# Performance work log

Measured on AMD Instinct MI355X. Metric: run time of the kernel, lower is better.

The kernel has to match this reference:

```python
import jax, jax.numpy as jnp
import numpy as np

B, S, D = 2, 2048, 2560
H, DH = 32, 80           # heads, head_size = D // H
RD = 32                  # rotary_dim (partial RoPE)
NI = 10240               # n_inner = 4 * n_embd
EPS = 1e-5
ROPE_BASE = 10000.0


def setup_inputs() -> dict:
    key = jax.random.key(0)
    ks = jax.random.split(key, 12)
    sd = 0.02
    inp = {
        "position_ids": jnp.broadcast_to(jnp.arange(S, dtype=jnp.int64), (B, S)),
        "hidden_states": jax.random.normal(ks[0], (B, S, D), jnp.float32),
        "ln_g": jnp.ones((D,), jnp.float32),
        "ln_b": jnp.zeros((D,), jnp.float32),
        "wqkv": jax.random.normal(ks[1], (D, 3 * D), jnp.float32) * sd,
        "bqkv": jnp.zeros((3 * D,), jnp.float32),
        "wout": jax.random.normal(ks[2], (D, D), jnp.float32) * sd,
        "bout": jnp.zeros((D,), jnp.float32),
        "wfc1": jax.random.normal(ks[3], (D, NI), jnp.float32) * sd,
        "bfc1": jnp.zeros((NI,), jnp.float32),
        "wfc2": jax.random.normal(ks[4], (NI, D), jnp.float32) * sd,
        "bfc2": jnp.zeros((D,), jnp.float32),
    }
    return inp


def _rope_neox(x, positions):
    # x: [B,S,H,DH]; apply neox-style rotary to first RD dims only
    half = RD // 2
    inv_freq = 1.0 / (ROPE_BASE ** (jnp.arange(0, RD, 2, dtype=jnp.float32) / RD))  # [half]
    ang = positions.astype(jnp.float32)[..., None] * inv_freq                        # [B,S,half]
    cos = jnp.cos(ang)[:, :, None, :]  # [B,S,1,half]
    sin = jnp.sin(ang)[:, :, None, :]
    x1 = x[..., :half]
    x2 = x[..., half:RD]
    rot = jnp.concatenate([x1 * cos - x2 * sin, x2 * cos + x1 * sin], axis=-1)
    return jnp.concatenate([rot, x[..., RD:]], axis=-1)


def reference(position_ids, hidden_states, ln_g, ln_b, wqkv, bqkv, wout, bout,
              wfc1, bfc1, wfc2, bfc2):
    residual = hidden_states
    # LayerNorm
    mu = jnp.mean(hidden_states, axis=-1, keepdims=True)
    var = jnp.mean(jnp.square(hidden_states - mu), axis=-1, keepdims=True)
    x = (hidden_states - mu) * jax.lax.rsqrt(var + EPS) * ln_g + ln_b

    # QKV projection
    qkv = x @ wqkv + bqkv
    q, k, v = jnp.split(qkv, 3, axis=-1)
    q = q.reshape(B, S, H, DH)
    k = k.reshape(B, S, H, DH)
    v = v.reshape(B, S, H, DH)

    # partial RoPE (neox style) on q and k
    q = _rope_neox(q, position_ids)
    k = _rope_neox(k, position_ids)

    # causal attention
    scale = DH ** -0.5
    scores = jnp.einsum("bqhd,bkhd->bhqk", q, k) * scale
    causal = jnp.tril(jnp.ones((S, S), jnp.bool_))
    scores = jnp.where(causal, scores, jnp.finfo(scores.dtype).min)
    probs = jax.nn.softmax(scores, axis=-1)
    attn = jnp.einsum("bhqk,bkhd->bqhd", probs, v).reshape(B, S, D)
    attn_out = attn @ wout + bout

    # MLP (gelu_new = tanh-approx gelu) on the SAME normed x (parallel residual)
    mlp = jax.nn.gelu(x @ wfc1 + bfc1, approximate=True) @ wfc2 + bfc2

    return attn_out + mlp + residual
```

## Files before the change

### kernel.cpp

```cpp
#include <hip/hip_runtime.h>

#define SS   2048
#define DD   2560
#define HH   32
#define DHH  80
#define DPAD 96
#define NII  10240
#define NTOK 4096

typedef __attribute__((ext_vector_type(8))) __bf16 bf16x8;
typedef __attribute__((ext_vector_type(4))) float  f32x4;

__device__ __forceinline__ float bf2f(unsigned short h) {
  union { unsigned u; float f; } c; c.u = ((unsigned)h) << 16; return c.f;
}
__device__ __forceinline__ unsigned short f2bf(float f) {
  union { float f; unsigned u; } c; c.f = f;
  unsigned r = c.u + 0x7FFFu + ((c.u >> 16) & 1u);
  return (unsigned short)(r >> 16);
}

__device__ __forceinline__ void gl_lds16(const void* gptr, void* lptr) {
  __builtin_amdgcn_global_load_lds((__attribute__((address_space(1))) void*)gptr,
                                   (__attribute__((address_space(3))) void*)lptr,
                                   16, 0, 0);
}

__global__ __launch_bounds__(256) void wt_transpose(const float* __restrict__ W,
                                                    unsigned short* __restrict__ Wt,
                                                    int K, int N) {
  __shared__ float tile[32][33];
  const int tx = threadIdx.x & 31, ty = threadIdx.x >> 5;
  const int n0 = blockIdx.x * 32, k0 = blockIdx.y * 32;
#pragma unroll
  for (int i = 0; i < 32; i += 8)
    tile[ty + i][tx] = W[(size_t)(k0 + ty + i) * N + n0 + tx];
  __syncthreads();
#pragma unroll
  for (int i = 0; i < 32; i += 8)
    Wt[(size_t)(n0 + ty + i) * K + k0 + tx] = f2bf(tile[tx][ty + i]);
}

__global__ __launch_bounds__(256) void ln_kernel(const float* __restrict__ X,
                                                 const float* __restrict__ G,
                                                 const float* __restrict__ Bb,
                                                 unsigned short* __restrict__ Xo) {
  const int row = blockIdx.x;
  const float4* xr = (const float4*)(X + (size_t)row * DD);
  float s = 0.f, ss = 0.f;
  for (int i = threadIdx.x; i < DD / 4; i += 256) {
    float4 v = xr[i];
    s  += v.x + v.y + v.z + v.w;
    ss += v.x * v.x + v.y * v.y + v.z * v.z + v.w * v.w;
  }
#pragma unroll
  for (int o = 32; o > 0; o >>= 1) { s += __shfl_down(s, o, 64); ss += __shfl_down(ss, o, 64); }
  __shared__ float red[8];
  const int w = threadIdx.x >> 6;
  if ((threadIdx.x & 63) == 0) { red[w] = s; red[4 + w] = ss; }
  __syncthreads();
  if (threadIdx.x == 0) {
    float ts  = red[0] + red[1] + red[2] + red[3];
    float tss = red[4] + red[5] + red[6] + red[7];
    float mu  = ts * (1.f / DD);
    float var = tss * (1.f / DD) - mu * mu;
    red[0] = mu; red[1] = rsqrtf(var + 1e-5f);
  }
  __syncthreads();
  const float mu = red[0], rstd = red[1];
  const float4* gr = (const float4*)G;
  const float4* br = (const float4*)Bb;
  for (int i = threadIdx.x; i < DD / 4; i += 256) {
    float4 v = xr[i], g = gr[i], b = br[i];
    ushort4 o;
    o.x = f2bf((v.x - mu) * rstd * g.x + b.x);
    o.y = f2bf((v.y - mu) * rstd * g.y + b.y);
    o.z = f2bf((v.z - mu) * rstd * g.z + b.z);
    o.w = f2bf((v.w - mu) * rstd * g.w + b.w);
    *(ushort4*)&Xo[(size_t)row * DD + i * 4] = o;
  }
}

__global__ __launch_bounds__(256) void rope_kernel(const unsigned short* __restrict__ qkv,
                                                   unsigned short* __restrict__ Qp,
                                                   unsigned short* __restrict__ Kp,
                                                   unsigned short* __restrict__ Vt) {
  const int tok = blockIdx.x;
  const int b = tok / SS, s = tok % SS;
  __shared__ float cs[16], sn[16];
  if (threadIdx.x < 16) {
    float inv = powf(10000.f, -(float)threadIdx.x / 16.f);
    float ang = (float)s * inv;
    cs[threadIdx.x] = cosf(ang);
    sn[threadIdx.x] = sinf(ang);
  }
  __syncthreads();
  const unsigned short* row = qkv + (size_t)tok * (3 * DD);
  for (int idx = threadIdx.x; idx < 2 * HH * DPAD; idx += 256) {
    const int which = idx / (HH * DPAD);
    const int rrem  = idx % (HH * DPAD);
    const int h = rrem / DPAD, d = rrem % DPAD;
    float val = 0.f;
    if (d < DHH) {
      const unsigned short* base = row + which * DD + h * DHH;
      if (d < 16) {
        float x1 = bf2f(base[d]), x2 = bf2f(base[d + 16]);
        val = x1 * cs[d] - x2 * sn[d];
      } else if (d < 32) {
        int i2 = d - 16;
        float x1 = bf2f(base[i2]), x2 = bf2f(base[d]);
        val = x2 * cs[i2] + x1 * sn[i2];
      } else {
        val = bf2f(base[d]);
      }
    }
    unsigned short* outp = which ? Kp : Qp;
    outp[(((size_t)b * HH + h) * SS + s) * DPAD + d] = f2bf(val);
  }
  for (int idx = threadIdx.x; idx < DD; idx += 256) {
    const int h = idx / DHH, d = idx % DHH;
    Vt[(((size_t)b * HH + h) * DHH + d) * SS + s] = row[2 * DD + idx];
  }
}

__global__ __launch_bounds__(128) void attn_kernel(const unsigned short* __restrict__ Qp,
                                                   const unsigned short* __restrict__ Kp,
                                                   const unsigned short* __restrict__ Vt,
                                                   unsigned short* __restrict__ O) {
  const int bid = blockIdx.x;
  const int bh = bid & 63;
  const int p = 63 - (bid >> 6);
  const int w = threadIdx.x >> 6;
  const int tile = p * 2 + w;
  const int lane = threadIdx.x & 63;
  const int lr = lane & 15, lg = lane >> 4;
  const int q0 = tile * 16;
  const unsigned short* Qh = Qp + (size_t)bh * SS * DPAD;
  const unsigned short* Kh = Kp + (size_t)bh * SS * DPAD;
  const unsigned short* Vh = Vt + (size_t)bh * DHH * SS;
  __shared__ __align__(16) char Plds[2][2048];
  char* Pb = Plds[w];

  bf16x8 qf[3];
#pragma unroll
  for (int c = 0; c < 3; ++c)
    qf[c] = *(const bf16x8*)&Qh[(size_t)(q0 + lr) * DPAD + c * 32 + lg * 8];

  f32x4 oacc[5];
#pragma unroll
  for (int d = 0; d < 5; ++d) oacc[d] = (f32x4){0.f, 0.f, 0.f, 0.f};
  float mrow[4], lrow[4];
#pragma unroll
  for (int r = 0; r < 4; ++r) { mrow[r] = -1e30f; lrow[r] = 0.f; }

  const float scl = 0.11180339887498949f;
  const int nt = q0 / 64 + 1;
  for (int t = 0; t < nt; ++t) {
    const int kv0 = t * 64;
    f32x4 s0 = (f32x4){0.f, 0.f, 0.f, 0.f};
    f32x4 s1 = (f32x4){0.f, 0.f, 0.f, 0.f};
    f32x4 s2 = (f32x4){0.f, 0.f, 0.f, 0.f};
    f32x4 s3 = (f32x4){0.f, 0.f, 0.f, 0.f};
#pragma unroll
    for (int c = 0; c < 3; ++c) {
      bf16x8 k0 = *(const bf16x8*)&Kh[(size_t)(kv0 +      lr) * DPAD + c * 32 + lg * 8];
      bf16x8 k1 = *(const bf16x8*)&Kh[(size_t)(kv0 + 16 + lr) * DPAD + c * 32 + lg * 8];
      bf16x8 k2 = *(const bf16x8*)&Kh[(size_t)(kv0 + 32 + lr) * DPAD + c * 32 + lg * 8];
      bf16x8 k3 = *(const bf16x8*)&Kh[(size_t)(kv0 + 48 + lr) * DPAD + c * 32 + lg * 8];
      s0 = __builtin_amdgcn_mfma_f32_16x16x32_bf16(qf[c], k0, s0, 0, 0, 0);
      s1 = __builtin_amdgcn_mfma_f32_16x16x32_bf16(qf[c], k1, s1, 0, 0, 0);
      s2 = __builtin_amdgcn_mfma_f32_16x16x32_bf16(qf[c], k2, s2, 0, 0, 0);
      s3 = __builtin_amdgcn_mfma_f32_16x16x32_bf16(qf[c], k3, s3, 0, 0, 0);
    }
    float pv0[4], pv1[4], pv2[4], pv3[4], mx[4];
    bool need = false;
#pragma unroll
    for (int r = 0; r < 4; ++r) {
      const int qr = q0 + lg * 4 + r;
      float a0 = (kv0 +      lr > qr) ? -1e30f : s0[r] * scl;
      float a1 = (kv0 + 16 + lr > qr) ? -1e30f : s1[r] * scl;
      float a2 = (kv0 + 32 + lr > qr) ? -1e30f : s2[r] * scl;
      float a3 = (kv0 + 48 + lr > qr) ? -1e30f : s3[r] * scl;
      pv0[r] = a0; pv1[r] = a1; pv2[r] = a2; pv3[r] = a3;
      float m = fmaxf(fmaxf(a0, a1), fmaxf(a2, a3));
#pragma unroll
      for (int mk = 1; mk < 16; mk <<= 1) m = fmaxf(m, __shfl_xor(m, mk, 64));
      mx[r] = m;
      need = need || (m > mrow[r] + 8.f);
    }
    if (__ballot(need)) {
#pragma unroll
      for (int r = 0; r < 4; ++r) {
        float mnew = fmaxf(mrow[r], mx[r]);
        float resc = __expf(mrow[r] - mnew);
        lrow[r] *= resc;
#pragma unroll
        for (int d = 0; d < 5; ++d) oacc[d][r] *= resc;
        mrow[r] = mnew;
      }
    }
#pragma unroll
    for (int r = 0; r < 4; ++r) {
      const int row = lg * 4 + r;
      const int swz = (row & 7) << 4;
      float p0 = __expf(pv0[r] - mrow[r]);
      float p1 = __expf(pv1[r] - mrow[r]);
      float p2 = __expf(pv2[r] - mrow[r]);
      float p3 = __expf(pv3[r] - mrow[r]);
      *(unsigned short*)(Pb + row * 128 + ((( 0 + lr) * 2) ^ swz)) = f2bf(p0);
      *(unsigned short*)(Pb + row * 128 + (((16 + lr) * 2) ^ swz)) = f2bf(p1);
      *(unsigned short*)(Pb + row * 128 + (((32 + lr) * 2) ^ swz)) = f2bf(p2);
      *(unsigned short*)(Pb + row * 128 + (((48 + lr) * 2) ^ swz)) = f2bf(p3);
      float rs = (p0 + p1) + (p2 + p3);
#pragma unroll
      for (int mk = 1; mk < 16; mk <<= 1) rs += __shfl_xor(rs, mk, 64);
      lrow[r] += rs;
    }
    asm volatile("s_waitcnt lgkmcnt(0)" ::: "memory");
    const int rswz = (lr & 7) << 4;
    bf16x8 pa0 = *(const bf16x8*)(Pb + lr * 128 + ((lg * 16) ^ rswz));
    bf16x8 pa1 = *(const bf16x8*)(Pb + lr * 128 + ((64 + lg * 16) ^ rswz));
#pragma unroll
    for (int d = 0; d < 5; ++d) {
      bf16x8 v0 = *(const bf16x8*)&Vh[(size_t)(d * 16 + lr) * SS + kv0 + lg * 8];
      bf16x8 v1 = *(const bf16x8*)&Vh[(size_t)(d * 16 + lr) * SS + kv0 + 32 + lg * 8];
      oacc[d] = __builtin_amdgcn_mfma_f32_16x16x32_bf16(pa0, v0, oacc[d], 0, 0, 0);
      oacc[d] = __builtin_amdgcn_mfma_f32_16x16x32_bf16(pa1, v1, oacc[d], 0, 0, 0);
    }
  }
  const int b = bh >> 5, h = bh & 31;
#pragma unroll
  for (int r = 0; r < 4; ++r) {
    const int qr = q0 + lg * 4 + r;
    const float inv = 1.f / lrow[r];
#pragma unroll
    for (int d = 0; d < 5; ++d)
      O[(size_t)(b * SS + qr) * DD + h * DHH + d * 16 + lr] = f2bf(oacc[d][r] * inv);
  }
}

__device__ __forceinline__ float gelu_f(float x) {
  float x3 = x * x * x;
  return 0.5f * x * (1.f + tanhf(0.7978845608028654f * (x + 0.044715f * x3)));
}

template <int MODE>
__global__ __launch_bounds__(512, 2) void gemm256(const unsigned short* __restrict__ A,
                                                  const unsigned short* __restrict__ Bt,
                                                  const float* __restrict__ bias,
                                                  void* __restrict__ Cout,
                                                  const unsigned short* __restrict__ addb,
                                                  const float* __restrict__ addf,
                                                  int M, int N, int K, int nby) {
  __shared__ __align__(16) char lds[131072];

  const int bid = blockIdx.x;
  const int by = bid % nby, bx = bid / nby;
  const int m0 = by * 256, n0 = bx * 256;

  const int tid = threadIdx.x;
  const int w = tid >> 6, lane = tid & 63;
  const int lr = lane & 15, lg = lane >> 4;
  const int wm = w >> 2, wn = w & 3;

  const int srow = w * 16 + (lane >> 3);
  const int scol = ((lane & 7) ^ ((lane >> 3) & 7)) * 8;
  const unsigned short* pA = A  + (size_t)(m0 + srow) * K + scol;
  const unsigned short* pB = Bt + (size_t)(n0 + srow) * K + scol;
  const int wdst = w * 2048;

  const int rdA = wm * 16384 + lr * 128;
  const int rdB = 65536 + (wn >> 1) * 16384 + ((wn & 1) * 64 + lr) * 128;
  const int sl0 = ((lg) ^ (lr & 7)) << 4;
  const int sl1 = ((4 + lg) ^ (lr & 7)) << 4;

  f32x4 acc[8][4];
#pragma unroll
  for (int i = 0; i < 8; ++i)
#pragma unroll
    for (int j = 0; j < 4; ++j) acc[i][j] = (f32x4){0.f, 0.f, 0.f, 0.f};

  const int nt = K >> 6;

#define RA(BUF, m, kh) (*(const bf16x8*)(lds + (BUF) + rdA + (m) * 2048 + ((kh) ? sl1 : sl0)))
#define RB(BUF, n, kh) (*(const bf16x8*)(lds + (BUF) + rdB + (n) * 2048 + ((kh) ? sl1 : sl0)))
#define STGA(dt, h, DST)                                                       \
  { const unsigned short* s_ = pA + (size_t)(dt) * 64 + (size_t)(h) * 128 * K; \
    gl_lds16(s_,                 lds + (DST) + wdst);                          \
    gl_lds16(s_ + (size_t)8 * K, lds + (DST) + wdst + 1024); }
#define STGB(dt, h, DST)                                                       \
  { const unsigned short* s_ = pB + (size_t)(dt) * 64 + (size_t)(h) * 128 * K; \
    gl_lds16(s_,                 lds + 65536 + (DST) + wdst);                  \
    gl_lds16(s_ + (size_t)8 * K, lds + 65536 + (DST) + wdst + 1024); }
#define BARR __builtin_amdgcn_s_barrier()
#define MFMA8x2(AV, BV, MB, NB)                                              \
  __builtin_amdgcn_s_setprio(1);                                             \
  _Pragma("unroll") for (int kh_ = 0; kh_ < 2; ++kh_)                        \
  _Pragma("unroll") for (int m_ = 0; m_ < 4; ++m_)                           \
  _Pragma("unroll") for (int n_ = 0; n_ < 2; ++n_)                           \
    acc[(MB) + m_][(NB) + n_] = __builtin_amdgcn_mfma_f32_16x16x32_bf16(     \
        AV[m_][kh_], BV[n_][kh_], acc[(MB) + m_][(NB) + n_], 0, 0, 0);       \
  __builtin_amdgcn_s_setprio(0);

  STGA(0, 0, 0);
  STGA(0, 1, 16384);
  STGB(0, 0, 0);
  STGB(0, 1, 16384);
  STGA(1, 0, 32768);
  STGA(1, 1, 32768 + 16384);
  STGB(1, 0, 32768);
  asm volatile("s_waitcnt vmcnt(6)" ::: "memory");
  BARR;
  __builtin_amdgcn_sched_barrier(0);

  for (int t = 0; t < nt; t += 2) {
    const bool more = (t + 2 < nt);
    bf16x8 avL[4][2], avH[4][2], bvL[2][2], bvH[2][2];

#pragma unroll
    for (int m_ = 0; m_ < 4; ++m_) { avL[m_][0] = RA(0, m_, 0); avL[m_][1] = RA(0, m_, 1); }
#pragma unroll
    for (int n_ = 0; n_ < 2; ++n_) { bvL[n_][0] = RB(0, n_, 0); bvL[n_][1] = RB(0, n_, 1); }
    STGB(1, 1, 32768 + 16384);
    BARR;
    MFMA8x2(avL, bvL, 0, 0);
    BARR;
#pragma unroll
    for (int m_ = 0; m_ < 4; ++m_) { avH[m_][0] = RA(0, 4 + m_, 0); avH[m_][1] = RA(0, 4 + m_, 1); }
    BARR;
    MFMA8x2(avH, bvL, 4, 0);
    BARR;
#pragma unroll
    for (int n_ = 0; n_ < 2; ++n_) { bvH[n_][0] = RB(0, 2 + n_, 0); bvH[n_][1] = RB(0, 2 + n_, 1); }
    if (more) STGA(2, 0, 0);
    BARR;
    MFMA8x2(avH, bvH, 4, 2);
    BARR;
    if (more) STGA(2, 1, 16384);
    BARR;
    MFMA8x2(avL, bvH, 0, 2);
    if (more) { asm volatile("s_waitcnt vmcnt(4)" ::: "memory"); }
    else      { asm volatile("s_waitcnt vmcnt(0)" ::: "memory"); }
    BARR;
    __builtin_amdgcn_sched_barrier(0);

#pragma unroll
    for (int m_ = 0; m_ < 4; ++m_) { avL[m_][0] = RA(32768, m_, 0); avL[m_][1] = RA(32768, m_, 1); }
#pragma unroll
    for (int n_ = 0; n_ < 2; ++n_) { bvL[n_][0] = RB(32768, n_, 0); bvL[n_][1] = RB(32768, n_, 1); }
    if (more) STGB(2, 0, 0);
    BARR;
    MFMA8x2(avL, bvL, 0, 0);
    BARR;
#pragma unroll
    for (int m_ = 0; m_ < 4; ++m_) { avH[m_][0] = RA(32768, 4 + m_, 0); avH[m_][1] = RA(32768, 4 + m_, 1); }
    if (more) STGB(2, 1, 16384);
    BARR;
    MFMA8x2(avH, bvL, 4, 0);
    BARR;
#pragma unroll
    for (int n_ = 0; n_ < 2; ++n_) { bvH[n_][0] = RB(32768, 2 + n_, 0); bvH[n_][1] = RB(32768, 2 + n_, 1); }
    if (more) STGA(3, 0, 32768);
    BARR;
    MFMA8x2(avH, bvH, 4, 2);
    BARR;
    if (more) { STGA(3, 1, 32768 + 16384); STGB(3, 0, 32768); }
    BARR;
    MFMA8x2(avL, bvH, 0, 2);
    if (more) { asm volatile("s_waitcnt vmcnt(6)" ::: "memory"); }
    BARR;
    __builtin_amdgcn_sched_barrier(0);

    pA += 128; pB += 128;
  }
#undef RA
#undef RB
#undef STGA
#undef STGB
#undef BARR
#undef MFMA8x2

#pragma unroll
  for (int m = 0; m < 8; ++m) {
    const int rb = m0 + wm * 128 + m * 16 + lg * 4;
#pragma unroll
    for (int n = 0; n < 4; ++n) {
      const int col = n0 + wn * 64 + n * 16 + lr;
      const float bv = bias[col];
#pragma unroll
      for (int r = 0; r < 4; ++r) {
        const size_t idx = (size_t)(rb + r) * N + col;
        float v = acc[m][n][r] + bv;
        if (MODE == 2) v = gelu_f(v);
        if (MODE == 3) {
          ((float*)Cout)[idx] = v + bf2f(addb[idx]) + addf[idx];
        } else {
          ((unsigned short*)Cout)[idx] = f2bf(v);
        }
      }
    }
  }
}

extern "C" void kernel_launch(void* const* d_in, const int* in_sizes, int n_in,
                              void* d_out, int out_size, void* d_ws, size_t ws_size,
                              hipStream_t stream) {
  (void)in_sizes; (void)n_in; (void)out_size; (void)ws_size;
  const float* hidden = (const float*)d_in[1];
  const float* ln_g = (const float*)d_in[2];
  const float* ln_b = (const float*)d_in[3];
  const float* wqkv = (const float*)d_in[4];
  const float* bqkv = (const float*)d_in[5];
  const float* wout = (const float*)d_in[6];
  const float* bout = (const float*)d_in[7];
  const float* wfc1 = (const float*)d_in[8];
  const float* bfc1 = (const float*)d_in[9];
  const float* wfc2 = (const float*)d_in[10];
  const float* bfc2 = (const float*)d_in[11];
  float* out = (float*)d_out;

  char* ws = (char*)d_ws;
  size_t off = 0;
  auto alloc = [&](size_t bytes) -> void* {
    void* p = ws + off;
    off += (bytes + 255) & ~(size_t)255;
    return p;
  };
  unsigned short* wqkvT = (unsigned short*)alloc((size_t)3 * DD * DD * 2);
  unsigned short* woutT = (unsigned short*)alloc((size_t)DD * DD * 2);
  unsigned short* wfc1T = (unsigned short*)alloc((size_t)NII * DD * 2);
  unsigned short* wfc2T = (unsigned short*)alloc((size_t)DD * NII * 2);
  unsigned short* xln   = (unsigned short*)alloc((size_t)NTOK * DD * 2);
  unsigned short* regA  = (unsigned short*)alloc((size_t)NTOK * NII * 2);
  unsigned short* Qp    = (unsigned short*)alloc((size_t)2 * HH * SS * DPAD * 2);
  unsigned short* Kp    = (unsigned short*)alloc((size_t)2 * HH * SS * DPAD * 2);
  unsigned short* Vt    = (unsigned short*)alloc((size_t)2 * HH * DHH * SS * 2);
  unsigned short* Obuf  = (unsigned short*)alloc((size_t)NTOK * DD * 2);
  unsigned short* qkvbuf   = regA;
  unsigned short* h1       = regA;
  unsigned short* attnproj = Qp;

  wt_transpose<<<dim3(3 * DD / 32, DD / 32), 256, 0, stream>>>(wqkv, wqkvT, DD, 3 * DD);
  wt_transpose<<<dim3(DD / 32, DD / 32), 256, 0, stream>>>(wout, woutT, DD, DD);
  wt_transpose<<<dim3(NII / 32, DD / 32), 256, 0, stream>>>(wfc1, wfc1T, DD, NII);
  wt_transpose<<<dim3(DD / 32, NII / 32), 256, 0, stream>>>(wfc2, wfc2T, NII, DD);
  ln_kernel<<<NTOK, 256, 0, stream>>>(hidden, ln_g, ln_b, xln);
  gemm256<0><<<dim3((3 * DD / 256) * (NTOK / 256)), 512, 0, stream>>>(
      xln, wqkvT, bqkv, qkvbuf, nullptr, nullptr, NTOK, 3 * DD, DD, NTOK / 256);
  rope_kernel<<<NTOK, 256, 0, stream>>>(qkvbuf, Qp, Kp, Vt);
  attn_kernel<<<dim3(4096), 128, 0, stream>>>(Qp, Kp, Vt, Obuf);
  gemm256<0><<<dim3((DD / 256) * (NTOK / 256)), 512, 0, stream>>>(
      Obuf, woutT, bout, attnproj, nullptr, nullptr, NTOK, DD, DD, NTOK / 256);
  gemm256<2><<<dim3((NII / 256) * (NTOK / 256)), 512, 0, stream>>>(
      xln, wfc1T, bfc1, h1, nullptr, nullptr, NTOK, NII, DD, NTOK / 256);
  gemm256<3><<<dim3((DD / 256) * (NTOK / 256)), 512, 0, stream>>>(
      h1, wfc2T, bfc2, out, attnproj, hidden, NTOK, DD, NII, NTOK / 256);
}
```

Measured before the change: 1.302 ms.

## Quantize QKV and output projection GEMMs to int8 with per-row/column scales

Replaces the bf16 QKV and attention-output projection GEMMs with an int8 MFMA GEMM. Weights get per-output-column absmax scales and activations get per-row absmax scales, with dequantization folded into the epilogue. This targets double-rate int8 matrix throughput and halves operand bandwidth. It adds colmax, quantize and rowquant passes and lowers numerical accuracy, which the tolerance may not accept.

```diff
diff --git a/kernel.cpp b/kernel.cpp
--- a/kernel.cpp
+++ b/kernel.cpp
@@ -10,6 +10,7 @@
 
 typedef __attribute__((ext_vector_type(8))) __bf16 bf16x8;
 typedef __attribute__((ext_vector_type(4))) float  f32x4;
+typedef __attribute__((ext_vector_type(4))) int    i32x4;
 
 __device__ __forceinline__ float bf2f(unsigned short h) {
   union { unsigned u; float f; } c; c.u = ((unsigned)h) << 16; return c.f;
@@ -24,6 +25,17 @@
   __builtin_amdgcn_global_load_lds((__attribute__((address_space(1))) void*)gptr,
                                    (__attribute__((address_space(3))) void*)lptr,
                                    16, 0, 0);
+}
+
+__global__ __launch_bounds__(256) void colmax_kernel(const float* __restrict__ W,
+                                                     float* __restrict__ rawmax,
+                                                     int K, int N) {
+  const int n = blockIdx.x * 256 + threadIdx.x;
+  const int kc = K >> 3;
+  const int k0 = blockIdx.y * kc, k1 = k0 + kc;
+  float m = 0.f;
+  for (int k = k0; k < k1; ++k) m = fmaxf(m, fabsf(W[(size_t)k * N + n]));
+  atomicMax((unsigned*)&rawmax[n], __float_as_uint(m));
 }
 
 __global__ __launch_bounds__(256) void wt_transpose(const float* __restrict__ W,
@@ -39,6 +51,65 @@
 #pragma unroll
   for (int i = 0; i < 32; i += 8)
     Wt[(size_t)(n0 + ty + i) * K + k0 + tx] = f2bf(tile[tx][ty + i]);
+}
+
+__global__ __launch_bounds__(256) void wt_q8(const float* __restrict__ W,
+                                             signed char* __restrict__ Wt8,
+                                             const float* __restrict__ rawmax,
+                                             int K, int N) {
+  __shared__ float tile[32][33];
+  const int tx = threadIdx.x & 31, ty = threadIdx.x >> 5;
+  const int n0 = blockIdx.x * 32, k0 = blockIdx.y * 32;
+#pragma unroll
+  for (int i = 0; i < 32; i += 8)
+    tile[ty + i][tx] = W[(size_t)(k0 + ty + i) * N + n0 + tx];
+  __syncthreads();
+#pragma unroll
+  for (int i = 0; i < 32; i += 8) {
+    const int n = n0 + ty + i;
+    const float inv = 127.f / fmaxf(rawmax[n], 1e-20f);
+    float q = rintf(tile[tx][ty + i] * inv);
+    q = fminf(fmaxf(q, -127.f), 127.f);
+    Wt8[(size_t)n * K + k0 + tx] = (signed char)q;
+  }
+}
+
+__global__ __launch_bounds__(256) void rowquant(const unsigned short* __restrict__ in,
+                                                signed char* __restrict__ outq,
+                                                float* __restrict__ srow, int Kd) {
+  const int row = blockIdx.x;
+  const unsigned short* r = in + (size_t)row * Kd;
+  float m = 0.f;
+  for (int i = threadIdx.x; i < Kd / 4; i += 256) {
+    ushort4 v = *(const ushort4*)&r[i * 4];
+    m = fmaxf(m, fabsf(bf2f(v.x)));
+    m = fmaxf(m, fabsf(bf2f(v.y)));
+    m = fmaxf(m, fabsf(bf2f(v.z)));
+    m = fmaxf(m, fabsf(bf2f(v.w)));
+  }
+#pragma unroll
+  for (int o = 32; o > 0; o >>= 1) m = fmaxf(m, __shfl_down(m, o, 64));
+  __shared__ float red[4];
+  if ((threadIdx.x & 63) == 0) red[threadIdx.x >> 6] = m;
+  __syncthreads();
+  if (threadIdx.x == 0) {
+    float t = fmaxf(fmaxf(red[0], red[1]), fmaxf(red[2], red[3]));
+    t = fmaxf(t, 1e-20f);
+    red[0] = 127.f / t;
+    srow[row] = t / 127.f;
+  }
+  __syncthreads();
+  const float inv = red[0];
+  signed char* o = outq + (size_t)row * Kd;
+  for (int i = threadIdx.x; i < Kd / 4; i += 256) {
+    ushort4 v = *(const ushort4*)&r[i * 4];
+    char4 q;
+    q.x = (signed char)fminf(fmaxf(rintf(bf2f(v.x) * inv), -127.f), 127.f);
+    q.y = (signed char)fminf(fmaxf(rintf(bf2f(v.y) * inv), -127.f), 127.f);
+    q.z = (signed char)fminf(fmaxf(rintf(bf2f(v.z) * inv), -127.f), 127.f);
+    q.w = (signed char)fminf(fmaxf(rintf(bf2f(v.w) * inv), -127.f), 127.f);
+    *(char4*)&o[i * 4] = q;
+  }
 }
 
 __global__ __launch_bounds__(256) void ln_kernel(const float* __restrict__ X,
@@ -402,6 +473,158 @@
   }
 }
 
+__global__ __launch_bounds__(512, 2) void gemm256_i8(const signed char* __restrict__ A,
+                                                     const signed char* __restrict__ Bt,
+                                                     const float* __restrict__ sA,
+                                                     const float* __restrict__ rawB,
+                                                     const float* __restrict__ bias,
+                                                     unsigned short* __restrict__ Cout,
+                                                     int M, int N, int K, int nby) {
+  __shared__ __align__(16) char lds[131072];
+
+  const int bid = blockIdx.x;
+  const int by = bid % nby, bx = bid / nby;
+  const int m0 = by * 256, n0 = bx * 256;
+
+  const int tid = threadIdx.x;
+  const int w = tid >> 6, lane = tid & 63;
+  const int lr = lane & 15, lg = lane >> 4;
+  const int wm = w >> 2, wn = w & 3;
+
+  const int srow = w * 16 + (lane >> 3);
+  const int scol = ((lane & 7) ^ ((lane >> 3) & 7)) * 16;
+  const signed char* pA = A  + (size_t)(m0 + srow) * K + scol;
+  const signed char* pB = Bt + (size_t)(n0 + srow) * K + scol;
+  const int wdst = w * 2048;
+
+  const int rdA = wm * 16384 + lr * 128;
+  const int rdB = 65536 + (wn >> 1) * 16384 + ((wn & 1) * 64 + lr) * 128;
+  const int sl0 = ((lg) ^ (lr & 7)) << 4;
+  const int sl1 = ((4 + lg) ^ (lr & 7)) << 4;
+
+  i32x4 acc[8][4];
+#pragma unroll
+  for (int i = 0; i < 8; ++i)
+#pragma unroll
+    for (int j = 0; j < 4; ++j) acc[i][j] = (i32x4){0, 0, 0, 0};
+
+  const int nt = K >> 7;
+
+#define RAI(BUF, m, kh) (*(const i32x4*)(lds + (BUF) + rdA + (m) * 2048 + ((kh) ? sl1 : sl0)))
+#define RBI(BUF, n, kh) (*(const i32x4*)(lds + (BUF) + rdB + (n) * 2048 + ((kh) ? sl1 : sl0)))
+#define STGAI(dt, h, DST)                                                       \
+  { const signed char* s_ = pA + (size_t)(dt) * 128 + (size_t)(h) * 128 * K;    \
+    gl_lds16(s_,                 lds + (DST) + wdst);                           \
+    gl_lds16(s_ + (size_t)8 * K, lds + (DST) + wdst + 1024); }
+#define STGBI(dt, h, DST)                                                       \
+  { const signed char* s_ = pB + (size_t)(dt) * 128 + (size_t)(h) * 128 * K;    \
+    gl_lds16(s_,                 lds + 65536 + (DST) + wdst);                   \
+    gl_lds16(s_ + (size_t)8 * K, lds + 65536 + (DST) + wdst + 1024); }
+#define BARRI __builtin_amdgcn_s_barrier()
+#define MFMAI8x2(AV, BV, MB, NB)                                             \
+  __builtin_amdgcn_s_setprio(1);                                             \
+  _Pragma("unroll") for (int kh_ = 0; kh_ < 2; ++kh_)                        \
+  _Pragma("unroll") for (int m_ = 0; m_ < 4; ++m_)                           \
+  _Pragma("unroll") for (int n_ = 0; n_ < 2; ++n_)                           \
+    acc[(MB) + m_][(NB) + n_] = __builtin_amdgcn_mfma_i32_16x16x64_i8(       \
+        AV[m_][kh_], BV[n_][kh_], acc[(MB) + m_][(NB) + n_], 0, 0, 0);       \
+  __builtin_amdgcn_s_setprio(0);
+
+  STGAI(0, 0, 0);
+  STGAI(0, 1, 16384);
+  STGBI(0, 0, 0);
+  STGBI(0, 1, 16384);
+  STGAI(1, 0, 32768);
+  STGAI(1, 1, 32768 + 16384);
+  STGBI(1, 0, 32768);
+  asm volatile("s_waitcnt vmcnt(6)" ::: "memory");
+  BARRI;
+  __builtin_amdgcn_sched_barrier(0);
+
+  for (int t = 0; t < nt; t += 2) {
+    const bool more = (t + 2 < nt);
+    i32x4 avL[4][2], avH[4][2], bvL[2][2], bvH[2][2];
+
+#pragma unroll
+    for (int m_ = 0; m_ < 4; ++m_) { avL[m_][0] = RAI(0, m_, 0); avL[m_][1] = RAI(0, m_, 1); }
+#pragma unroll
+    for (int n_ = 0; n_ < 2; ++n_) { bvL[n_][0] = RBI(0, n_, 0); bvL[n_][1] = RBI(0, n_, 1); }
+    STGBI(1, 1, 32768 + 16384);
+    BARRI;
+    MFMAI8x2(avL, bvL, 0, 0);
+    BARRI;
+#pragma unroll
+    for (int m_ = 0; m_ < 4; ++m_) { avH[m_][0] = RAI(0, 4 + m_, 0); avH[m_][1] = RAI(0, 4 + m_, 1); }
+    BARRI;
+    MFMAI8x2(avH, bvL, 4, 0);
+    BARRI;
+#pragma unroll
+    for (int n_ = 0; n_ < 2; ++n_) { bvH[n_][0] = RBI(0, 2 + n_, 0); bvH[n_][1] = RBI(0, 2 + n_, 1); }
+    if (more) STGAI(2, 0, 0);
+    BARRI;
+    MFMAI8x2(avH, bvH, 4, 2);
+    BARRI;
+    if (more) STGAI(2, 1, 16384);
+    BARRI;
+    MFMAI8x2(avL, bvH, 0, 2);
+    if (more) { asm volatile("s_waitcnt vmcnt(4)" ::: "memory"); }
+    else      { asm volatile("s_waitcnt vmcnt(0)" ::: "memory"); }
+    BARRI;
+    __builtin_amdgcn_sched_barrier(0);
+
+#pragma unroll
+    for (int m_ = 0; m_ < 4; ++m_) { avL[m_][0] = RAI(32768, m_, 0); avL[m_][1] = RAI(32768, m_, 1); }
+#pragma unroll
+    for (int n_ = 0; n_ < 2; ++n_) { bvL[n_][0] = RBI(32768, n_, 0); bvL[n_][1] = RBI(32768, n_, 1); }
+    if (more) STGBI(2, 0, 0);
+    BARRI;
+    MFMAI8x2(avL, bvL, 0, 0);
+    BARRI;
+#pragma unroll
+    for (int m_ = 0; m_ < 4; ++m_) { avH[m_][0] = RAI(32768, 4 + m_, 0); avH[m_][1] = RAI(32768, 4 + m_, 1); }
+    if (more) STGBI(2, 1, 16384);
+    BARRI;
+    MFMAI8x2(avH, bvL, 4, 0);
+    BARRI;
+#pragma unroll
+    for (int n_ = 0; n_ < 2; ++n_) { bvH[n_][0] = RBI(32768, 2 + n_, 0); bvH[n_][1] = RBI(32768, 2 + n_, 1); }
+    if (more) STGAI(3, 0, 32768);
+    BARRI;
+    MFMAI8x2(avH, bvH, 4, 2);
+    BARRI;
+    if (more) { STGAI(3, 1, 32768 + 16384); STGBI(3, 0, 32768); }
+    BARRI;
+    MFMAI8x2(avL, bvH, 0, 2);
+    if (more) { asm volatile("s_waitcnt vmcnt(6)" ::: "memory"); }
+    BARRI;
+    __builtin_amdgcn_sched_barrier(0);
+
+    pA += 256; pB += 256;
+  }
+#undef RAI
+#undef RBI
+#undef STGAI
+#undef STGBI
+#undef BARRI
+#undef MFMAI8x2
+
+#pragma unroll
+  for (int m = 0; m < 8; ++m) {
+    const int rb = m0 + wm * 128 + m * 16 + lg * 4;
+    float sr0 = sA[rb], sr1 = sA[rb + 1], sr2 = sA[rb + 2], sr3 = sA[rb + 3];
+#pragma unroll
+    for (int n = 0; n < 4; ++n) {
+      const int col = n0 + wn * 64 + n * 16 + lr;
+      const float sc = rawB[col] * (1.f / 127.f);
+      const float bv = bias[col];
+      Cout[(size_t)(rb + 0) * N + col] = f2bf((float)acc[m][n][0] * sr0 * sc + bv);
+      Cout[(size_t)(rb + 1) * N + col] = f2bf((float)acc[m][n][1] * sr1 * sc + bv);
+      Cout[(size_t)(rb + 2) * N + col] = f2bf((float)acc[m][n][2] * sr2 * sc + bv);
+      Cout[(size_t)(rb + 3) * N + col] = f2bf((float)acc[m][n][3] * sr3 * sc + bv);
+    }
+  }
+}
+
 extern "C" void kernel_launch(void* const* d_in, const int* in_sizes, int n_in,
                               void* d_out, int out_size, void* d_ws, size_t ws_size,
                               hipStream_t stream) {
@@ -426,11 +649,17 @@
     off += (bytes + 255) & ~(size_t)255;
     return p;
   };
-  unsigned short* wqkvT = (unsigned short*)alloc((size_t)3 * DD * DD * 2);
-  unsigned short* woutT = (unsigned short*)alloc((size_t)DD * DD * 2);
+  signed char*  wqkvT8 = (signed char*)alloc((size_t)3 * DD * DD);
+  signed char*  woutT8 = (signed char*)alloc((size_t)DD * DD);
   unsigned short* wfc1T = (unsigned short*)alloc((size_t)NII * DD * 2);
   unsigned short* wfc2T = (unsigned short*)alloc((size_t)DD * NII * 2);
   unsigned short* xln   = (unsigned short*)alloc((size_t)NTOK * DD * 2);
+  signed char*  xq      = (signed char*)alloc((size_t)NTOK * DD);
+  signed char*  oq      = (signed char*)alloc((size_t)NTOK * DD);
+  float* rawqkv = (float*)alloc((size_t)3 * DD * 4);
+  float* rawout = (float*)alloc((size_t)DD * 4);
+  float* sx     = (float*)alloc((size_t)NTOK * 4);
+  float* so     = (float*)alloc((size_t)NTOK * 4);
   unsigned short* regA  = (unsigned short*)alloc((size_t)NTOK * NII * 2);
   unsigned short* Qp    = (unsigned short*)alloc((size_t)2 * HH * SS * DPAD * 2);
   unsigned short* Kp    = (unsigned short*)alloc((size_t)2 * HH * SS * DPAD * 2);
@@ -440,17 +669,23 @@
   unsigned short* h1       = regA;
   unsigned short* attnproj = Qp;
 
-  wt_transpose<<<dim3(3 * DD / 32, DD / 32), 256, 0, stream>>>(wqkv, wqkvT, DD, 3 * DD);
-  wt_transpose<<<dim3(DD / 32, DD / 32), 256, 0, stream>>>(wout, woutT, DD, DD);
+  hipMemsetAsync(rawqkv, 0, (size_t)(3 * DD + DD) * 4, stream);
+
+  colmax_kernel<<<dim3(3 * DD / 256, 8), 256, 0, stream>>>(wqkv, rawqkv, DD, 3 * DD);
+  colmax_kernel<<<dim3(DD / 256, 8), 256, 0, stream>>>(wout, rawout, DD, DD);
+  wt_q8<<<dim3(3 * DD / 32, DD / 32), 256, 0, stream>>>(wqkv, wqkvT8, rawqkv, DD, 3 * DD);
+  wt_q8<<<dim3(DD / 32, DD / 32), 256, 0, stream>>>(wout, woutT8, rawout, DD, DD);
   wt_transpose<<<dim3(NII / 32, DD / 32), 256, 0, stream>>>(wfc1, wfc1T, DD, NII);
   wt_transpose<<<dim3(DD / 32, NII / 32), 256, 0, stream>>>(wfc2, wfc2T, NII, DD);
   ln_kernel<<<NTOK, 256, 0, stream>>>(hidden, ln_g, ln_b, xln);
-  gemm256<0><<<dim3((3 * DD / 256) * (NTOK / 256)), 512, 0, stream>>>(
-      xln, wqkvT, bqkv, qkvbuf, nullptr, nullptr, NTOK, 3 * DD, DD, NTOK / 256);
+  rowquant<<<NTOK, 256, 0, stream>>>(xln, xq, sx, DD);
+  gemm256_i8<<<dim3((3 * DD / 256) * (NTOK / 256)), 512, 0, stream>>>(
+      xq, wqkvT8, sx, rawqkv, bqkv, qkvbuf, NTOK, 3 * DD, DD, NTOK / 256);
   rope_kernel<<<NTOK, 256, 0, stream>>>(qkvbuf, Qp, Kp, Vt);
   attn_kernel<<<dim3(4096), 128, 0, stream>>>(Qp, Kp, Vt, Obuf);
-  gemm256<0><<<dim3((DD / 256) * (NTOK / 256)), 512, 0, stream>>>(
-      Obuf, woutT, bout, attnproj, nullptr, nullptr, NTOK, DD, DD, NTOK / 256);
+  rowquant<<<NTOK, 256, 0, stream>>>(Obuf, oq, so, DD);
+  gemm256_i8<<<dim3((DD / 256) * (NTOK / 256)), 512, 0, stream>>>(
+      oq, woutT8, so, rawout, bout, attnproj, NTOK, DD, DD, NTOK / 256);
   gemm256<2><<<dim3((NII / 256) * (NTOK / 256)), 512, 0, stream>>>(
       xln, wfc1T, bfc1, h1, nullptr, nullptr, NTOK, NII, DD, NTOK / 256);
   gemm256<3><<<dim3((DD / 256) * (NTOK / 256)), 512, 0, stream>>>(
```

Result: slower. 1.487 ms (+14.2%).

## Replace direct global-to-LDS loads with register-staged double-buffered GEMM pipeline

Applied to the files above, without the earlier changes.

The GEMM main loop stops using global_load_lds with a hand-scheduled barrier and vmcnt pipeline. Instead it loads the next K-tile into registers, stores it to a swizzled, double-buffered LDS slot, and synchronises with __syncthreads around each tile's MFMA work. Launch bounds drop to one block per CU, which gives more registers for the staging buffers. This simplifies scheduling but adds VGPR pressure and an LDS write pass, and it may lose the fine-grained overlap of the original interleaved schedule.

```diff
diff --git a/kernel.cpp b/kernel.cpp
--- a/kernel.cpp
+++ b/kernel.cpp
@@ -18,12 +18,6 @@
   union { float f; unsigned u; } c; c.f = f;
   unsigned r = c.u + 0x7FFFu + ((c.u >> 16) & 1u);
   return (unsigned short)(r >> 16);
-}
-
-__device__ __forceinline__ void gl_lds16(const void* gptr, void* lptr) {
-  __builtin_amdgcn_global_load_lds((__attribute__((address_space(1))) void*)gptr,
-                                   (__attribute__((address_space(3))) void*)lptr,
-                                   16, 0, 0);
 }
 
 __global__ __launch_bounds__(256) void wt_transpose(const float* __restrict__ W,
@@ -245,7 +239,7 @@
 }
 
 template <int MODE>
-__global__ __launch_bounds__(512, 2) void gemm256(const unsigned short* __restrict__ A,
+__global__ __launch_bounds__(512, 1) void gemm256(const unsigned short* __restrict__ A,
                                                   const unsigned short* __restrict__ Bt,
                                                   const float* __restrict__ bias,
                                                   void* __restrict__ Cout,
@@ -263,14 +257,20 @@
   const int lr = lane & 15, lg = lane >> 4;
   const int wm = w >> 2, wn = w & 3;
 
-  const int srow = w * 16 + (lane >> 3);
-  const int scol = ((lane & 7) ^ ((lane >> 3) & 7)) * 8;
-  const unsigned short* pA = A  + (size_t)(m0 + srow) * K + scol;
-  const unsigned short* pB = Bt + (size_t)(n0 + srow) * K + scol;
-  const int wdst = w * 2048;
+  const int srow = w * 32 + (lane >> 3);
+  const int sslot = lane & 7;
+  const unsigned short* pA = A  + (size_t)(m0 + srow) * K + sslot * 8;
+  const unsigned short* pB = Bt + (size_t)(n0 + srow) * K + sslot * 8;
+
+  int wadr[4];
+#pragma unroll
+  for (int i = 0; i < 4; ++i) {
+    const int row = srow + i * 8;
+    wadr[i] = (row >> 7) * 16384 + (row & 127) * 128 + ((sslot ^ (row & 7)) << 4);
+  }
 
   const int rdA = wm * 16384 + lr * 128;
-  const int rdB = 65536 + (wn >> 1) * 16384 + ((wn & 1) * 64 + lr) * 128;
+  const int rdB = (wn >> 1) * 16384 + ((wn & 1) * 64 + lr) * 128;
   const int sl0 = ((lg) ^ (lr & 7)) << 4;
   const int sl1 = ((4 + lg) ^ (lr & 7)) << 4;
 
@@ -282,17 +282,16 @@
 
   const int nt = K >> 6;
 
-#define RA(BUF, m, kh) (*(const bf16x8*)(lds + (BUF) + rdA + (m) * 2048 + ((kh) ? sl1 : sl0)))
-#define RB(BUF, n, kh) (*(const bf16x8*)(lds + (BUF) + rdB + (n) * 2048 + ((kh) ? sl1 : sl0)))
-#define STGA(dt, h, DST)                                                       \
-  { const unsigned short* s_ = pA + (size_t)(dt) * 64 + (size_t)(h) * 128 * K; \
-    gl_lds16(s_,                 lds + (DST) + wdst);                          \
-    gl_lds16(s_ + (size_t)8 * K, lds + (DST) + wdst + 1024); }
-#define STGB(dt, h, DST)                                                       \
-  { const unsigned short* s_ = pB + (size_t)(dt) * 64 + (size_t)(h) * 128 * K; \
-    gl_lds16(s_,                 lds + 65536 + (DST) + wdst);                  \
-    gl_lds16(s_ + (size_t)8 * K, lds + 65536 + (DST) + wdst + 1024); }
-#define BARR __builtin_amdgcn_s_barrier()
+  bf16x8 ra[4], rb[4];
+
+#define ISSUE(t)                                                        \
+  { const unsigned short* qa = pA + (size_t)(t) * 64;                   \
+    const unsigned short* qb = pB + (size_t)(t) * 64;                   \
+    _Pragma("unroll") for (int i = 0; i < 4; ++i) {                     \
+      ra[i] = *(const bf16x8*)(qa + (size_t)i * 8 * K);                 \
+      rb[i] = *(const bf16x8*)(qb + (size_t)i * 8 * K); } }
+#define RA(AB, m, kh) (*(const bf16x8*)(lds + (AB) + rdA + (m) * 2048 + ((kh) ? sl1 : sl0)))
+#define RB(BB, n, kh) (*(const bf16x8*)(lds + (BB) + rdB + (n) * 2048 + ((kh) ? sl1 : sl0)))
 #define MFMA8x2(AV, BV, MB, NB)                                              \
   __builtin_amdgcn_s_setprio(1);                                             \
   _Pragma("unroll") for (int kh_ = 0; kh_ < 2; ++kh_)                        \
@@ -302,94 +301,49 @@
         AV[m_][kh_], BV[n_][kh_], acc[(MB) + m_][(NB) + n_], 0, 0, 0);       \
   __builtin_amdgcn_s_setprio(0);
 
-  STGA(0, 0, 0);
-  STGA(0, 1, 16384);
-  STGB(0, 0, 0);
-  STGB(0, 1, 16384);
-  STGA(1, 0, 32768);
-  STGA(1, 1, 32768 + 16384);
-  STGB(1, 0, 32768);
-  asm volatile("s_waitcnt vmcnt(6)" ::: "memory");
-  BARR;
-  __builtin_amdgcn_sched_barrier(0);
-
-  for (int t = 0; t < nt; t += 2) {
-    const bool more = (t + 2 < nt);
-    bf16x8 avL[4][2], avH[4][2], bvL[2][2], bvH[2][2];
-
-#pragma unroll
-    for (int m_ = 0; m_ < 4; ++m_) { avL[m_][0] = RA(0, m_, 0); avL[m_][1] = RA(0, m_, 1); }
-#pragma unroll
-    for (int n_ = 0; n_ < 2; ++n_) { bvL[n_][0] = RB(0, n_, 0); bvL[n_][1] = RB(0, n_, 1); }
-    STGB(1, 1, 32768 + 16384);
-    BARR;
-    MFMA8x2(avL, bvL, 0, 0);
-    BARR;
-#pragma unroll
-    for (int m_ = 0; m_ < 4; ++m_) { avH[m_][0] = RA(0, 4 + m_, 0); avH[m_][1] = RA(0, 4 + m_, 1); }
-    BARR;
-    MFMA8x2(avH, bvL, 4, 0);
-    BARR;
-#pragma unroll
-    for (int n_ = 0; n_ < 2; ++n_) { bvH[n_][0] = RB(0, 2 + n_, 0); bvH[n_][1] = RB(0, 2 + n_, 1); }
-    if (more) STGA(2, 0, 0);
-    BARR;
-    MFMA8x2(avH, bvH, 4, 2);
-    BARR;
-    if (more) STGA(2, 1, 16384);
-    BARR;
-    MFMA8x2(avL, bvH, 0, 2);
-    if (more) { asm volatile("s_waitcnt vmcnt(4)" ::: "memory"); }
-    else      { asm volatile("s_waitcnt vmcnt(0)" ::: "memory"); }
-    BARR;
-    __builtin_amdgcn_sched_barrier(0);
-
-#pragma unroll
-    for (int m_ = 0; m_ < 4; ++m_) { avL[m_][0] = RA(32768, m_, 0); avL[m_][1] = RA(32768, m_, 1); }
-#pragma unroll
-    for (int n_ = 0; n_ < 2; ++n_) { bvL[n_][0] = RB(32768, n_, 0); bvL[n_][1] = RB(32768, n_, 1); }
-    if (more) STGB(2, 0, 0);
-    BARR;
-    MFMA8x2(avL, bvL, 0, 0);
-    BARR;
-#pragma unroll
-    for (int m_ = 0; m_ < 4; ++m_) { avH[m_][0] = RA(32768, 4 + m_, 0); avH[m_][1] = RA(32768, 4 + m_, 1); }
-    if (more) STGB(2, 1, 16384);
-    BARR;
-    MFMA8x2(avH, bvL, 4, 0);
-    BARR;
-#pragma unroll
-    for (int n_ = 0; n_ < 2; ++n_) { bvH[n_][0] = RB(32768, 2 + n_, 0); bvH[n_][1] = RB(32768, 2 + n_, 1); }
-    if (more) STGA(3, 0, 32768);
-    BARR;
-    MFMA8x2(avH, bvH, 4, 2);
-    BARR;
-    if (more) { STGA(3, 1, 32768 + 16384); STGB(3, 0, 32768); }
-    BARR;
-    MFMA8x2(avL, bvH, 0, 2);
-    if (more) { asm volatile("s_waitcnt vmcnt(6)" ::: "memory"); }
-    BARR;
-    __builtin_amdgcn_sched_barrier(0);
-
-    pA += 128; pB += 128;
-  }
+  ISSUE(0);
+
+  for (int t = 0; t < nt; ++t) {
+    const int ab = (t & 1) * 32768;
+    const int bb = 65536 + ab;
+#pragma unroll
+    for (int i = 0; i < 4; ++i) *(bf16x8*)(lds + ab + wadr[i]) = ra[i];
+#pragma unroll
+    for (int i = 0; i < 4; ++i) *(bf16x8*)(lds + bb + wadr[i]) = rb[i];
+    __syncthreads();
+    if (t + 1 < nt) ISSUE(t + 1);
+    {
+      bf16x8 avL[4][2], avH[4][2], bvL[2][2], bvH[2][2];
+#pragma unroll
+      for (int m_ = 0; m_ < 4; ++m_) { avL[m_][0] = RA(ab, m_, 0); avL[m_][1] = RA(ab, m_, 1); }
+#pragma unroll
+      for (int n_ = 0; n_ < 2; ++n_) { bvL[n_][0] = RB(bb, n_, 0); bvL[n_][1] = RB(bb, n_, 1); }
+      MFMA8x2(avL, bvL, 0, 0);
+#pragma unroll
+      for (int m_ = 0; m_ < 4; ++m_) { avH[m_][0] = RA(ab, 4 + m_, 0); avH[m_][1] = RA(ab, 4 + m_, 1); }
+      MFMA8x2(avH, bvL, 4, 0);
+#pragma unroll
+      for (int n_ = 0; n_ < 2; ++n_) { bvH[n_][0] = RB(bb, 2 + n_, 0); bvH[n_][1] = RB(bb, 2 + n_, 1); }
+      MFMA8x2(avH, bvH, 4, 2);
+      MFMA8x2(avL, bvH, 0, 2);
+    }
+    __syncthreads();
+  }
+#undef ISSUE
 #undef RA
 #undef RB
-#undef STGA
-#undef STGB
-#undef BARR
 #undef MFMA8x2
 
 #pragma unroll
   for (int m = 0; m < 8; ++m) {
-    const int rb = m0 + wm * 128 + m * 16 + lg * 4;
+    const int rb2 = m0 + wm * 128 + m * 16 + lg * 4;
 #pragma unroll
     for (int n = 0; n < 4; ++n) {
       const int col = n0 + wn * 64 + n * 16 + lr;
       const float bv = bias[col];
 #pragma unroll
       for (int r = 0; r < 4; ++r) {
-        const size_t idx = (size_t)(rb + r) * N + col;
+        const size_t idx = (size_t)(rb2 + r) * N + col;
         float v = acc[m][n][r] + bv;
         if (MODE == 2) v = gelu_f(v);
         if (MODE == 3) {
```

Measured after the change: 2.037 ms. +56.4%, slower.

## Process two 16-row query groups per wave in attention to reuse K/V loads

Applied to the files above, without the earlier changes.

Each attention wave now handles 32 query rows (two 16-row MFMA groups) instead of 16, so every K and V fragment loaded from global memory feeds twice as many MFMAs. The grid is halved to match. This cuts redundant K/V traffic per query but raises register pressure (doubled accumulators and softmax state), reduces the number of blocks available for latency hiding, and makes the causal tail slightly coarser.

```diff
diff --git a/kernel.cpp b/kernel.cpp
--- a/kernel.cpp
+++ b/kernel.cpp
@@ -129,114 +129,138 @@
                                                    unsigned short* __restrict__ O) {
   const int bid = blockIdx.x;
   const int bh = bid & 63;
-  const int p = 63 - (bid >> 6);
+  const int p = 31 - (bid >> 6);
   const int w = threadIdx.x >> 6;
   const int tile = p * 2 + w;
   const int lane = threadIdx.x & 63;
   const int lr = lane & 15, lg = lane >> 4;
-  const int q0 = tile * 16;
+  const int q0 = tile * 32;
   const unsigned short* Qh = Qp + (size_t)bh * SS * DPAD;
   const unsigned short* Kh = Kp + (size_t)bh * SS * DPAD;
   const unsigned short* Vh = Vt + (size_t)bh * DHH * SS;
-  __shared__ __align__(16) char Plds[2][2048];
-  char* Pb = Plds[w];
-
-  bf16x8 qf[3];
-#pragma unroll
-  for (int c = 0; c < 3; ++c)
-    qf[c] = *(const bf16x8*)&Qh[(size_t)(q0 + lr) * DPAD + c * 32 + lg * 8];
-
-  f32x4 oacc[5];
-#pragma unroll
-  for (int d = 0; d < 5; ++d) oacc[d] = (f32x4){0.f, 0.f, 0.f, 0.f};
-  float mrow[4], lrow[4];
-#pragma unroll
-  for (int r = 0; r < 4; ++r) { mrow[r] = -1e30f; lrow[r] = 0.f; }
+  __shared__ __align__(16) char Plds[2][2][2048];
+
+  bf16x8 qf[2][3];
+#pragma unroll
+  for (int g = 0; g < 2; ++g)
+#pragma unroll
+    for (int c = 0; c < 3; ++c)
+      qf[g][c] = *(const bf16x8*)&Qh[(size_t)(q0 + g * 16 + lr) * DPAD + c * 32 + lg * 8];
+
+  f32x4 oacc[2][5];
+#pragma unroll
+  for (int g = 0; g < 2; ++g)
+#pragma unroll
+    for (int d = 0; d < 5; ++d) oacc[g][d] = (f32x4){0.f, 0.f, 0.f, 0.f};
+  float mrow[2][4], lrow[2][4];
+#pragma unroll
+  for (int g = 0; g < 2; ++g)
+#pragma unroll
+    for (int r = 0; r < 4; ++r) { mrow[g][r] = -1e30f; lrow[g][r] = 0.f; }
 
   const float scl = 0.11180339887498949f;
-  const int nt = q0 / 64 + 1;
+  const int nt = (q0 + 31) / 64 + 1;
   for (int t = 0; t < nt; ++t) {
     const int kv0 = t * 64;
-    f32x4 s0 = (f32x4){0.f, 0.f, 0.f, 0.f};
-    f32x4 s1 = (f32x4){0.f, 0.f, 0.f, 0.f};
-    f32x4 s2 = (f32x4){0.f, 0.f, 0.f, 0.f};
-    f32x4 s3 = (f32x4){0.f, 0.f, 0.f, 0.f};
+    f32x4 s[2][4];
+#pragma unroll
+    for (int g = 0; g < 2; ++g)
+#pragma unroll
+      for (int j = 0; j < 4; ++j) s[g][j] = (f32x4){0.f, 0.f, 0.f, 0.f};
 #pragma unroll
     for (int c = 0; c < 3; ++c) {
-      bf16x8 k0 = *(const bf16x8*)&Kh[(size_t)(kv0 +      lr) * DPAD + c * 32 + lg * 8];
-      bf16x8 k1 = *(const bf16x8*)&Kh[(size_t)(kv0 + 16 + lr) * DPAD + c * 32 + lg * 8];
-      bf16x8 k2 = *(const bf16x8*)&Kh[(size_t)(kv0 + 32 + lr) * DPAD + c * 32 + lg * 8];
-      bf16x8 k3 = *(const bf16x8*)&Kh[(size_t)(kv0 + 48 + lr) * DPAD + c * 32 + lg * 8];
-      s0 = __builtin_amdgcn_mfma_f32_16x16x32_bf16(qf[c], k0, s0, 0, 0, 0);
-      s1 = __builtin_amdgcn_mfma_f32_16x16x32_bf16(qf[c], k1, s1, 0, 0, 0);
-      s2 = __builtin_amdgcn_mfma_f32_16x16x32_bf16(qf[c], k2, s2, 0, 0, 0);
-      s3 = __builtin_amdgcn_mfma_f32_16x16x32_bf16(qf[c], k3, s3, 0, 0, 0);
-    }
-    float pv0[4], pv1[4], pv2[4], pv3[4], mx[4];
+      bf16x8 kf[4];
+#pragma unroll
+      for (int j = 0; j < 4; ++j)
+        kf[j] = *(const bf16x8*)&Kh[(size_t)(kv0 + j * 16 + lr) * DPAD + c * 32 + lg * 8];
+#pragma unroll
+      for (int g = 0; g < 2; ++g)
+#pragma unroll
+        for (int j = 0; j < 4; ++j)
+          s[g][j] = __builtin_amdgcn_mfma_f32_16x16x32_bf16(qf[g][c], kf[j], s[g][j], 0, 0, 0);
+    }
+    float pv[2][4][4], mx[2][4];
     bool need = false;
 #pragma unroll
-    for (int r = 0; r < 4; ++r) {
-      const int qr = q0 + lg * 4 + r;
-      float a0 = (kv0 +      lr > qr) ? -1e30f : s0[r] * scl;
-      float a1 = (kv0 + 16 + lr > qr) ? -1e30f : s1[r] * scl;
-      float a2 = (kv0 + 32 + lr > qr) ? -1e30f : s2[r] * scl;
-      float a3 = (kv0 + 48 + lr > qr) ? -1e30f : s3[r] * scl;
-      pv0[r] = a0; pv1[r] = a1; pv2[r] = a2; pv3[r] = a3;
-      float m = fmaxf(fmaxf(a0, a1), fmaxf(a2, a3));
-#pragma unroll
-      for (int mk = 1; mk < 16; mk <<= 1) m = fmaxf(m, __shfl_xor(m, mk, 64));
-      mx[r] = m;
-      need = need || (m > mrow[r] + 8.f);
+    for (int g = 0; g < 2; ++g) {
+#pragma unroll
+      for (int r = 0; r < 4; ++r) {
+        const int qr = q0 + g * 16 + lg * 4 + r;
+        float m = -1e30f;
+#pragma unroll
+        for (int j = 0; j < 4; ++j) {
+          float a = (kv0 + j * 16 + lr > qr) ? -1e30f : s[g][j][r] * scl;
+          pv[g][j][r] = a;
+          m = fmaxf(m, a);
+        }
+#pragma unroll
+        for (int mk = 1; mk < 16; mk <<= 1) m = fmaxf(m, __shfl_xor(m, mk, 64));
+        mx[g][r] = m;
+        need = need || (m > mrow[g][r] + 8.f);
+      }
     }
     if (__ballot(need)) {
 #pragma unroll
+      for (int g = 0; g < 2; ++g)
+#pragma unroll
+        for (int r = 0; r < 4; ++r) {
+          float mnew = fmaxf(mrow[g][r], mx[g][r]);
+          float resc = __expf(mrow[g][r] - mnew);
+          lrow[g][r] *= resc;
+#pragma unroll
+          for (int d = 0; d < 5; ++d) oacc[g][d][r] *= resc;
+          mrow[g][r] = mnew;
+        }
+    }
+#pragma unroll
+    for (int g = 0; g < 2; ++g) {
+      char* Pb = Plds[w][g];
+#pragma unroll
       for (int r = 0; r < 4; ++r) {
-        float mnew = fmaxf(mrow[r], mx[r]);
-        float resc = __expf(mrow[r] - mnew);
-        lrow[r] *= resc;
-#pragma unroll
-        for (int d = 0; d < 5; ++d) oacc[d][r] *= resc;
-        mrow[r] = mnew;
+        const int row = lg * 4 + r;
+        const int swz = (row & 7) << 4;
+        float rs = 0.f;
+#pragma unroll
+        for (int j = 0; j < 4; ++j) {
+          float pj = __expf(pv[g][j][r] - mrow[g][r]);
+          rs += pj;
+          *(unsigned short*)(Pb + row * 128 + (((j * 16 + lr) * 2) ^ swz)) = f2bf(pj);
+        }
+#pragma unroll
+        for (int mk = 1; mk < 16; mk <<= 1) rs += __shfl_xor(rs, mk, 64);
+        lrow[g][r] += rs;
       }
-    }
-#pragma unroll
-    for (int r = 0; r < 4; ++r) {
-      const int row = lg * 4 + r;
-      const int swz = (row & 7) << 4;
-      float p0 = __expf(pv0[r] - mrow[r]);
-      float p1 = __expf(pv1[r] - mrow[r]);
-      float p2 = __expf(pv2[r] - mrow[r]);
-      float p3 = __expf(pv3[r] - mrow[r]);
-      *(unsigned short*)(Pb + row * 128 + ((( 0 + lr) * 2) ^ swz)) = f2bf(p0);
-      *(unsigned short*)(Pb + row * 128 + (((16 + lr) * 2) ^ swz)) = f2bf(p1);
-      *(unsigned short*)(Pb + row * 128 + (((32 + lr) * 2) ^ swz)) = f2bf(p2);
-      *(unsigned short*)(Pb + row * 128 + (((48 + lr) * 2) ^ swz)) = f2bf(p3);
-      float rs = (p0 + p1) + (p2 + p3);
-#pragma unroll
-      for (int mk = 1; mk < 16; mk <<= 1) rs += __shfl_xor(rs, mk, 64);
-      lrow[r] += rs;
     }
     asm volatile("s_waitcnt lgkmcnt(0)" ::: "memory");
     const int rswz = (lr & 7) << 4;
-    bf16x8 pa0 = *(const bf16x8*)(Pb + lr * 128 + ((lg * 16) ^ rswz));
-    bf16x8 pa1 = *(const bf16x8*)(Pb + lr * 128 + ((64 + lg * 16) ^ rswz));
+    bf16x8 pa[2][2];
+#pragma unroll
+    for (int g = 0; g < 2; ++g) {
+      pa[g][0] = *(const bf16x8*)(Plds[w][g] + lr * 128 + ((lg * 16) ^ rswz));
+      pa[g][1] = *(const bf16x8*)(Plds[w][g] + lr * 128 + ((64 + lg * 16) ^ rswz));
+    }
 #pragma unroll
     for (int d = 0; d < 5; ++d) {
       bf16x8 v0 = *(const bf16x8*)&Vh[(size_t)(d * 16 + lr) * SS + kv0 + lg * 8];
       bf16x8 v1 = *(const bf16x8*)&Vh[(size_t)(d * 16 + lr) * SS + kv0 + 32 + lg * 8];
-      oacc[d] = __builtin_amdgcn_mfma_f32_16x16x32_bf16(pa0, v0, oacc[d], 0, 0, 0);
-      oacc[d] = __builtin_amdgcn_mfma_f32_16x16x32_bf16(pa1, v1, oacc[d], 0, 0, 0);
+#pragma unroll
+      for (int g = 0; g < 2; ++g) {
+        oacc[g][d] = __builtin_amdgcn_mfma_f32_16x16x32_bf16(pa[g][0], v0, oacc[g][d], 0, 0, 0);
+        oacc[g][d] = __builtin_amdgcn_mfma_f32_16x16x32_bf16(pa[g][1], v1, oacc[g][d], 0, 0, 0);
+      }
     }
   }
   const int b = bh >> 5, h = bh & 31;
 #pragma unroll
-  for (int r = 0; r < 4; ++r) {
-    const int qr = q0 + lg * 4 + r;
-    const float inv = 1.f / lrow[r];
-#pragma unroll
-    for (int d = 0; d < 5; ++d)
-      O[(size_t)(b * SS + qr) * DD + h * DHH + d * 16 + lr] = f2bf(oacc[d][r] * inv);
-  }
+  for (int g = 0; g < 2; ++g)
+#pragma unroll
+    for (int r = 0; r < 4; ++r) {
+      const int qr = q0 + g * 16 + lg * 4 + r;
+      const float inv = 1.f / lrow[g][r];
+#pragma unroll
+      for (int d = 0; d < 5; ++d)
+        O[(size_t)(b * SS + qr) * DD + h * DHH + d * 16 + lr] = f2bf(oacc[g][d][r] * inv);
+    }
 }
 
 __device__ __forceinline__ float gelu_f(float x) {
@@ -448,7 +472,7 @@
   gemm256<0><<<dim3((3 * DD / 256) * (NTOK / 256)), 512, 0, stream>>>(
       xln, wqkvT, bqkv, qkvbuf, nullptr, nullptr, NTOK, 3 * DD, DD, NTOK / 256);
   rope_kernel<<<NTOK, 256, 0, stream>>>(qkvbuf, Qp, Kp, Vt);
-  attn_kernel<<<dim3(4096), 128, 0, stream>>>(Qp, Kp, Vt, Obuf);
+  attn_kernel<<<dim3(2048), 128, 0, stream>>>(Qp, Kp, Vt, Obuf);
   gemm256<0><<<dim3((DD / 256) * (NTOK / 256)), 512, 0, stream>>>(
       Obuf, woutT, bout, attnproj, nullptr, nullptr, NTOK, DD, DD, NTOK / 256);
   gemm256<2><<<dim3((NII / 256) * (NTOK / 256)), 512, 0, stream>>>(
```

Result: faster. 1.220 ms, median of 2 (-6.3%).
